# Kernel tuning notes

Hardware: AMD Instinct MI355X
Metric: run time of the kernel (lower is better)

Reference implementation:

```python
import jax, jax.numpy as jnp
import numpy as np

B, L, D = 32, 512, 256
MAX_DUR = 8


def setup_inputs() -> dict:
    key = jax.random.key(0)
    k1, k2 = jax.random.split(key)
    hidden_phonems = jax.random.normal(k1, (B, L, D), dtype=jnp.float32)
    durations = jax.random.randint(k2, (B, L), 0, MAX_DUR, dtype=jnp.int32)
    return {"hidden_phonems": hidden_phonems, "durations": durations}


def reference(hidden_phonems, durations):
    # hidden_phonems: [B, L, D], durations: [B, L] int
    totals = jnp.sum(durations, axis=1)                    # [B] mel length per utterance
    max_T = int(jnp.max(totals))                           # batch-max padded length (matches torch)
    cum = jnp.cumsum(durations, axis=1)                    # [B, L] exclusive-of-next prefix sums
    t = jnp.arange(max_T, dtype=jnp.int32)                 # output frame positions
    # frame t belongs to the first phoneme whose cumulative duration exceeds t
    idx = jax.vmap(lambda c: jnp.searchsorted(c, t, side='right'))(cum)  # [B, max_T]
    idx = jnp.clip(idx, 0, hidden_phonems.shape[1] - 1)
    out = jnp.take_along_axis(hidden_phonems, idx[:, :, None], axis=1)   # [B, max_T, D]
    mask = (t[None, :] < totals[:, None])                  # zero out padding frames
    return out * mask[:, :, None].astype(out.dtype)
```

## Files before the change

### kernel.cpp

```cpp
#include <hip/hip_runtime.h>
#include <hip/hip_bf16.h>

#define B_SZ 32
#define L_SZ 512
#define D_SZ 256
#define PHON_BLOCKS (B_SZ * L_SZ / 4)
#define PAD_FRAMES_PER_BLOCK 16

__global__ void scan_kernel(const int* __restrict__ durations,
                            int* __restrict__ cum) {
    __shared__ int s[L_SZ];
    const int b = blockIdx.x;
    const int tid = threadIdx.x;

    s[tid] = durations[b * L_SZ + tid];
    __syncthreads();

    #pragma unroll
    for (int off = 1; off < L_SZ; off <<= 1) {
        int v = (tid >= off) ? s[tid - off] : 0;
        __syncthreads();
        s[tid] += v;
        __syncthreads();
    }

    cum[b * L_SZ + tid] = s[tid];
}

__global__ void __launch_bounds__(256)
expand_kernel(const float* __restrict__ hidden,
              const int* __restrict__ durations,
              const int* __restrict__ cum,
              float* __restrict__ out,
              int maxT, int padBlocksPerB) {
    const int tid  = threadIdx.x;
    const int lane = tid & 63;
    const int wave = tid >> 6;

    if (blockIdx.x < PHON_BLOCKS) {
        const int wid = blockIdx.x * 4 + wave;
        const int b = wid >> 9;
        const int l = wid & (L_SZ - 1);
        const int d = durations[b * L_SZ + l];
        if (d == 0) return;
        const int end   = cum[b * L_SZ + l];
        const int start = end - d;

        const float4* src =
            (const float4*)(hidden + ((size_t)(b * L_SZ + l)) * D_SZ);
        float4 v = src[lane];

        float4* dst =
            (float4*)(out + ((size_t)b * maxT + start) * D_SZ) + lane;
        #pragma unroll
        for (int j = 0; j < 7; ++j) {
            if (j < d) dst[j * 64] = v;
        }
    } else {
        const int pb   = blockIdx.x - PHON_BLOCKS;
        const int b    = pb / padBlocksPerB;
        const int tile = pb % padBlocksPerB;
        const int total = cum[b * L_SZ + (L_SZ - 1)];
        const int t0 = tile * PAD_FRAMES_PER_BLOCK;
        if (t0 + PAD_FRAMES_PER_BLOCK <= total) return;

        const float4 z = make_float4(0.f, 0.f, 0.f, 0.f);
        #pragma unroll
        for (int i = 0; i < 4; ++i) {
            const int t = t0 + wave * 4 + i;
            if (t >= total && t < maxT) {
                float4* dst = (float4*)(out + ((size_t)b * maxT + t) * D_SZ);
                dst[lane] = z;
            }
        }
    }
}

extern "C" void kernel_launch(void* const* d_in, const int* in_sizes, int n_in,
                              void* d_out, int out_size, void* d_ws, size_t ws_size,
                              hipStream_t stream) {
    const float* hidden = (const float*)d_in[0];
    const int* durations = (const int*)d_in[1];
    float* out = (float*)d_out;

    int* cum = (int*)d_ws;

    const int maxT = out_size / (B_SZ * D_SZ);
    const int padBlocksPerB = (maxT + PAD_FRAMES_PER_BLOCK - 1) / PAD_FRAMES_PER_BLOCK;
    const int grid = PHON_BLOCKS + B_SZ * padBlocksPerB;

    scan_kernel<<<B_SZ, L_SZ, 0, stream>>>(durations, cum);
    expand_kernel<<<grid, 256, 0, stream>>>(hidden, durations, cum, out,
                                            maxT, padBlocksPerB);
}
```

Measured before the change: 84.61 us.

## Fuse prefix-sum scan into expand kernel via per-wave redundant reduction

Drops the separate scan kernel and its workspace write. Each wave now loads its utterance's full duration row (2 KB), computes its own exclusive prefix with a masked per-lane sum plus a wave-wide xor-shuffle reduction, and picks its duration with a shuffle. The padding blocks likewise compute the row total themselves. This saves one kernel launch and the serial dependency between the kernels, at the cost of redundant row reads and reductions in every wave, which are mostly served from cache.

```diff
diff --git a/kernel.cpp b/kernel.cpp
--- a/kernel.cpp
+++ b/kernel.cpp
@@ -7,32 +7,11 @@
 #define PHON_BLOCKS (B_SZ * L_SZ / 4)
 #define PAD_FRAMES_PER_BLOCK 16
 
-__global__ void scan_kernel(const int* __restrict__ durations,
-                            int* __restrict__ cum) {
-    __shared__ int s[L_SZ];
-    const int b = blockIdx.x;
-    const int tid = threadIdx.x;
-
-    s[tid] = durations[b * L_SZ + tid];
-    __syncthreads();
-
-    #pragma unroll
-    for (int off = 1; off < L_SZ; off <<= 1) {
-        int v = (tid >= off) ? s[tid - off] : 0;
-        __syncthreads();
-        s[tid] += v;
-        __syncthreads();
-    }
-
-    cum[b * L_SZ + tid] = s[tid];
-}
-
 __global__ void __launch_bounds__(256)
-expand_kernel(const float* __restrict__ hidden,
-              const int* __restrict__ durations,
-              const int* __restrict__ cum,
-              float* __restrict__ out,
-              int maxT, int padBlocksPerB) {
+lr_kernel(const float* __restrict__ hidden,
+          const int* __restrict__ durations,
+          float* __restrict__ out,
+          int maxT, int padBlocksPerB) {
     const int tid  = threadIdx.x;
     const int lane = tid & 63;
     const int wave = tid >> 6;
@@ -41,14 +20,35 @@
         const int wid = blockIdx.x * 4 + wave;
         const int b = wid >> 9;
         const int l = wid & (L_SZ - 1);
-        const int d = durations[b * L_SZ + l];
+
+        const int4* drow = (const int4*)(durations + b * L_SZ);
+        const int4 a = drow[lane * 2];
+        const int4 c = drow[lane * 2 + 1];
+
+        const int base = lane * 8;
+        int s = 0;
+        s += (base + 0 < l) ? a.x : 0;
+        s += (base + 1 < l) ? a.y : 0;
+        s += (base + 2 < l) ? a.z : 0;
+        s += (base + 3 < l) ? a.w : 0;
+        s += (base + 4 < l) ? c.x : 0;
+        s += (base + 5 < l) ? c.y : 0;
+        s += (base + 6 < l) ? c.z : 0;
+        s += (base + 7 < l) ? c.w : 0;
+        #pragma unroll
+        for (int off = 32; off; off >>= 1) s += __shfl_xor(s, off, 64);
+        const int start = s;
+
+        const int k = l & 7;
+        const int pick =
+            (k < 4) ? ((k < 2) ? (k == 0 ? a.x : a.y) : (k == 2 ? a.z : a.w))
+                    : ((k < 6) ? (k == 4 ? c.x : c.y) : (k == 6 ? c.z : c.w));
+        const int d = __shfl(pick, l >> 3, 64);
         if (d == 0) return;
-        const int end   = cum[b * L_SZ + l];
-        const int start = end - d;
 
         const float4* src =
             (const float4*)(hidden + ((size_t)(b * L_SZ + l)) * D_SZ);
-        float4 v = src[lane];
+        const float4 v = src[lane];
 
         float4* dst =
             (float4*)(out + ((size_t)b * maxT + start) * D_SZ) + lane;
@@ -60,8 +60,16 @@
         const int pb   = blockIdx.x - PHON_BLOCKS;
         const int b    = pb / padBlocksPerB;
         const int tile = pb % padBlocksPerB;
-        const int total = cum[b * L_SZ + (L_SZ - 1)];
-        const int t0 = tile * PAD_FRAMES_PER_BLOCK;
+        const int t0   = tile * PAD_FRAMES_PER_BLOCK;
+
+        const int4* drow = (const int4*)(durations + b * L_SZ);
+        const int4 a = drow[lane * 2];
+        const int4 c = drow[lane * 2 + 1];
+        int s = a.x + a.y + a.z + a.w + c.x + c.y + c.z + c.w;
+        #pragma unroll
+        for (int off = 32; off; off >>= 1) s += __shfl_xor(s, off, 64);
+        const int total = s;
+
         if (t0 + PAD_FRAMES_PER_BLOCK <= total) return;
 
         const float4 z = make_float4(0.f, 0.f, 0.f, 0.f);
@@ -83,13 +91,10 @@
     const int* durations = (const int*)d_in[1];
     float* out = (float*)d_out;
 
-    int* cum = (int*)d_ws;
-
     const int maxT = out_size / (B_SZ * D_SZ);
     const int padBlocksPerB = (maxT + PAD_FRAMES_PER_BLOCK - 1) / PAD_FRAMES_PER_BLOCK;
     const int grid = PHON_BLOCKS + B_SZ * padBlocksPerB;
 
-    scan_kernel<<<B_SZ, L_SZ, 0, stream>>>(durations, cum);
-    expand_kernel<<<grid, 256, 0, stream>>>(hidden, durations, cum, out,
-                                            maxT, padBlocksPerB);
+    lr_kernel<<<grid, 256, 0, stream>>>(hidden, durations, out,
+                                        maxT, padBlocksPerB);
 }
```

New measurement: 82.86 us. 2.1% less time.
